# Performance work log

Measured on AMD Instinct MI355X. Metric: run time of the kernel, lower is better.

Reference implementation:

```python
import jax, jax.numpy as jnp
import numpy as np

N_NODES = 100000
N_EDGES = 1600000
IN_DIM = 128
OUT_DIM = 64


def setup_inputs() -> dict:
    key = jax.random.key(0)
    k1, k2, k3, k4, k5 = jax.random.split(key, 5)
    x = jax.random.normal(k1, (N_NODES, IN_DIM), dtype=jnp.float32)
    edge_index = jax.random.randint(k2, (2, N_EDGES), 0, N_NODES, dtype=jnp.int64)
    # xavier_uniform for Linear(in,out): bound = sqrt(6/(in+out))
    wb = float(np.sqrt(6.0 / (IN_DIM + OUT_DIM)))
    W = jax.random.uniform(k3, (OUT_DIM, IN_DIM), dtype=jnp.float32, minval=-wb, maxval=wb)
    # xavier_uniform on a.unsqueeze(0): fan_in=out_dim, fan_out=1
    ab = float(np.sqrt(6.0 / (OUT_DIM + 1)))
    a_src = jax.random.uniform(k4, (OUT_DIM,), dtype=jnp.float32, minval=-ab, maxval=b if (b := ab) else ab)
    a_dst = jax.random.uniform(k5, (OUT_DIM,), dtype=jnp.float32, minval=-ab, maxval=ab)
    return {"x": x, "edge_index": edge_index, "W": W, "a_src": a_src, "a_dst": a_dst}


def reference(x, edge_index, W, a_src, a_dst):
    # h = x @ W^T : [N, out_dim]
    h = x @ W.T
    src, dst = edge_index[0], edge_index[1]
    # per-node attention logits, gathered per edge (cheaper than gathering h twice for the dot)
    s_src = h @ a_src  # [N]
    s_dst = h @ a_dst  # [N]
    e = s_src[src] + s_dst[dst]  # [E]
    e = jnp.where(e >= 0, e, 0.2 * e)  # LeakyReLU(0.2)
    e = jnp.clip(e, -10.0, 10.0)
    alpha_num = jnp.exp(e)
    denom = jax.ops.segment_sum(alpha_num, dst, num_segments=N_NODES)  # [N]
    alpha = alpha_num / (denom[dst] + 1e-9)  # [E]; dropout is identity (eval / p=0)
    msgs = alpha[:, None] * h[src]  # [E, out_dim]
    out = jax.ops.segment_sum(msgs, dst, num_segments=N_NODES)  # [N, out_dim]
    return out
```

## Files before the change

### kernel.cpp

```cpp
#include <hip/hip_runtime.h>
#include <math.h>

#define NN 100000
#define NE 1600000
#define NBKT 391
#define LPS  (NBKT + 1)
#define EPB 2048
#define NPB ((NE + EPB - 1) / EPB)
#define TOTC (NBKT * NPB)
#define SBLK 2048
#define NSB ((TOTC + SBLK - 1) / SBLK)
#define LBUF 6144

typedef unsigned int uint;
typedef unsigned short ushort;
typedef __attribute__((ext_vector_type(8))) short bfx8;
typedef __attribute__((ext_vector_type(4))) float f32x4;

static __device__ __forceinline__ ushort f2bf(float f) {
  uint u = __float_as_uint(f);
  uint r = (u + 0x7fffu + ((u >> 16) & 1u)) >> 16;
  return (ushort)r;
}
static __device__ __forceinline__ float bf2f(ushort v) {
  return __uint_as_float((uint)v << 16);
}
static __device__ __forceinline__ bfx8 cvt8(float4 a, float4 b) {
  bfx8 r;
  r[0] = (short)f2bf(a.x); r[1] = (short)f2bf(a.y);
  r[2] = (short)f2bf(a.z); r[3] = (short)f2bf(a.w);
  r[4] = (short)f2bf(b.x); r[5] = (short)f2bf(b.y);
  r[6] = (short)f2bf(b.z); r[7] = (short)f2bf(b.w);
  return r;
}

__global__ __launch_bounds__(256) void k_h(
    const float* __restrict__ x, const float* __restrict__ W,
    const float* __restrict__ a_src, const float* __restrict__ a_dst,
    ushort* __restrict__ h16, float* __restrict__ ssrc, float* __restrict__ sdst)
{
  __shared__ __align__(16) ushort ws[64 * 128];
  const int t = threadIdx.x;
  const int base = blockIdx.x * 64;
  const float4* x4 = (const float4*)x;
  const float4* W4 = (const float4*)W;

#pragma unroll
  for (int q = 0; q < 8; ++q) {
    int f = q * 256 + t;
    int row = f >> 5, c4 = f & 31;
    float4 v = W4[f];
    ushort4 pk = make_ushort4(f2bf(v.x), f2bf(v.y), f2bf(v.z), f2bf(v.w));
    int byte = row * 256 + ((c4 * 8) ^ ((row & 7) << 4));
    *(ushort4*)((char*)ws + byte) = pk;
  }

  const int wid = t >> 6;
  const int lane = t & 63;
  const int lg = lane >> 4;
  const int lr = lane & 15;

  const int node = base + wid * 16 + lr;
  const bool ok = node < NN;
  const float4* xr = x4 + (size_t)node * 32;

  float4 xa[4][2];
#pragma unroll
  for (int ks = 0; ks < 4; ++ks) {
    xa[ks][0] = ok ? xr[ks * 8 + lg * 2]     : make_float4(0.f, 0.f, 0.f, 0.f);
    xa[ks][1] = ok ? xr[ks * 8 + lg * 2 + 1] : make_float4(0.f, 0.f, 0.f, 0.f);
  }
  __syncthreads();

  f32x4 acc[4];
#pragma unroll
  for (int ng = 0; ng < 4; ++ng) acc[ng] = (f32x4){0.f, 0.f, 0.f, 0.f};

#pragma unroll
  for (int ks = 0; ks < 4; ++ks) {
    int kb = ks * 64 + lg * 16;
    bfx8 af = cvt8(xa[ks][0], xa[ks][1]);
    bfx8 bfr[4];
#pragma unroll
    for (int ng = 0; ng < 4; ++ng) {
      int row = ng * 16 + lr;
      bfr[ng] = *(const bfx8*)((const char*)ws + row * 256 + (kb ^ ((row & 7) << 4)));
    }
#pragma unroll
    for (int ng = 0; ng < 4; ++ng)
      acc[ng] = __builtin_amdgcn_mfma_f32_16x16x32_bf16(af, bfr[ng], acc[ng], 0, 0, 0);
  }

  float as_[4], ad_[4];
#pragma unroll
  for (int ng = 0; ng < 4; ++ng) { as_[ng] = a_src[ng * 16 + lr]; ad_[ng] = a_dst[ng * 16 + lr]; }
#pragma unroll
  for (int r = 0; r < 4; ++r) {
    int nout = base + wid * 16 + lg * 4 + r;
    float ps = 0.f, pd = 0.f;
#pragma unroll
    for (int ng = 0; ng < 4; ++ng) { ps += acc[ng][r] * as_[ng]; pd += acc[ng][r] * ad_[ng]; }
#pragma unroll
    for (int m = 1; m < 16; m <<= 1) { ps += __shfl_xor(ps, m); pd += __shfl_xor(pd, m); }
    if (lr == 0 && nout < NN) { ssrc[nout] = ps; sdst[nout] = pd; }
    if (nout < NN) {
#pragma unroll
      for (int ng = 0; ng < 4; ++ng)
        h16[(size_t)nout * 64 + ng * 16 + lr] = f2bf(acc[ng][r]);
    }
  }
}

__global__ __launch_bounds__(512) void k_sort(const int* __restrict__ ei,
                                              const float* __restrict__ ssrc,
                                              int* __restrict__ cnt,
                                              int* __restrict__ lpre,
                                              int2* __restrict__ stage)
{
  __shared__ int hh[NBKT];
  __shared__ int sums[512];
  __shared__ int2 sbuf[EPB];
  const int t = threadIdx.x, c = blockIdx.x;
  for (int i = t; i < NBKT; i += 512) hh[i] = 0;
  __syncthreads();

  const int base = c * EPB;
  const int nloc = min(EPB, NE - base);
  int my_src[EPB / 512], my_dst[EPB / 512];
#pragma unroll
  for (int q = 0; q < EPB / 512; ++q) {
    int e = base + q * 512 + t;
    if (e < NE) {
      my_src[q] = ei[e];
      my_dst[q] = ei[NE + e];
      atomicAdd(&hh[my_dst[q] >> 8], 1);
    } else my_dst[q] = -1;
  }
  __syncthreads();

  int v = (t < NBKT) ? hh[t] : 0;
  sums[t] = v;
  __syncthreads();
  for (int off = 1; off < 512; off <<= 1) {
    int u = (t >= off) ? sums[t - off] : 0;
    __syncthreads();
    sums[t] += u;
    __syncthreads();
  }
  int ex = sums[t] - v;
  if (t < NBKT) {
    hh[t] = ex;
    lpre[c * LPS + t] = ex;
    cnt[t * NPB + c] = v;
  }
  if (t == 0) lpre[c * LPS + NBKT] = nloc;
  __syncthreads();

#pragma unroll
  for (int q = 0; q < EPB / 512; ++q) {
    if (my_dst[q] >= 0) {
      int dst = my_dst[q], src = my_src[q];
      int pos = atomicAdd(&hh[dst >> 8], 1);
      sbuf[pos] = make_int2(src | ((dst & 255) << 24), __float_as_int(ssrc[src]));
    }
  }
  __syncthreads();
#pragma unroll
  for (int q = 0; q < EPB / 512; ++q) {
    int i = q * 512 + t;
    if (i < nloc) stage[base + i] = sbuf[i];
  }
}

__global__ __launch_bounds__(256) void k_scanA(const int* __restrict__ cnt,
                                               int* __restrict__ partials)
{
  __shared__ int sm[256];
  int t = threadIdx.x, b = blockIdx.x;
  const int4* c4 = (const int4*)(cnt + b * SBLK + t * 8);
  int4 u = c4[0], v = c4[1];
  sm[t] = u.x + u.y + u.z + u.w + v.x + v.y + v.z + v.w;
  __syncthreads();
  for (int s = 128; s > 0; s >>= 1) { if (t < s) sm[t] += sm[t + s]; __syncthreads(); }
  if (t == 0) partials[b] = sm[0];
}

__global__ __launch_bounds__(256) void k_scanB(int* __restrict__ partials,
                                               int* __restrict__ boff,
                                               int* __restrict__ offsets)
{
  __shared__ int sm[256];
  int t = threadIdx.x;
  int v = (t < NSB) ? partials[t] : 0;
  sm[t] = v;
  __syncthreads();
  for (int off = 1; off < 256; off <<= 1) {
    int u = (t >= off) ? sm[t - off] : 0;
    __syncthreads();
    sm[t] += u;
    __syncthreads();
  }
  if (t < NSB) partials[t] = sm[t] - v;
  if (t == 0) { boff[NBKT] = NE; offsets[NN] = NE; }
}

__global__ __launch_bounds__(256) void k_scanC(int* __restrict__ cnt,
                                               const int* __restrict__ partials,
                                               int* __restrict__ boff)
{
  __shared__ int sm[256];
  int t = threadIdx.x, b = blockIdx.x;
  int base = b * SBLK + t * 8;
  int4* c4 = (int4*)(cnt + base);
  int4 u = c4[0], v = c4[1];
  int tot = u.x + u.y + u.z + u.w + v.x + v.y + v.z + v.w;
  sm[t] = tot;
  __syncthreads();
  for (int off = 1; off < 256; off <<= 1) {
    int w = (t >= off) ? sm[t - off] : 0;
    __syncthreads();
    sm[t] += w;
    __syncthreads();
  }
  int run = partials[b] + sm[t] - tot;
  int e[8] = {u.x, u.y, u.z, u.w, v.x, v.y, v.z, v.w};
  int ex[8];
#pragma unroll
  for (int k = 0; k < 8; ++k) { ex[k] = run; run += e[k]; }
#pragma unroll
  for (int k = 0; k < 8; ++k) {
    int idx = base + k;
    if (idx < TOTC && idx % NPB == 0) boff[idx / NPB] = ex[k];
  }
  c4[0] = make_int4(ex[0], ex[1], ex[2], ex[3]);
  c4[1] = make_int4(ex[4], ex[5], ex[6], ex[7]);
}

__global__ __launch_bounds__(512) void k_place(const int* __restrict__ boff,
                                               const int* __restrict__ cnt,
                                               const int* __restrict__ lpre,
                                               const int2* __restrict__ stage,
                                               const float* __restrict__ sdst,
                                               int* __restrict__ offsets,
                                               int2* __restrict__ csr)
{
  __shared__ int2 lbuf[LBUF];
  __shared__ int nh[256];
  __shared__ int cur[256];
  __shared__ float sdl[256];
  const int b = blockIdx.x, t = threadIdx.x;
  const int e_beg = boff[b], e_end = boff[b + 1];
  const int m = e_end - e_beg;

  for (int c = t; c < NPB; c += 512) {
    int lp = lpre[c * LPS + b];
    int lq = lpre[c * LPS + b + 1];
    int outp = cnt[b * NPB + c] - e_beg;
    int sin = c * EPB + lp;
    for (int k = 0; k < lq - lp; ++k) lbuf[outp + k] = stage[sin + k];
  }
  if (t < 256) {
    nh[t] = 0;
    int node = (b << 8) + t;
    sdl[t] = (node < NN) ? sdst[node] : 0.f;
  }
  __syncthreads();

  for (int i = t; i < m; i += 512)
    atomicAdd(&nh[((uint)lbuf[i].x) >> 24], 1);
  __syncthreads();
  int v0 = (t < 256) ? nh[t] : 0;
  for (int off = 1; off < 256; off <<= 1) {
    int u = (t >= off && t < 256) ? nh[t - off] : 0;
    __syncthreads();
    if (t < 256) nh[t] += u;
    __syncthreads();
  }
  if (t < 256) {
    int excl = nh[t] - v0;
    cur[t] = excl;
    int node = (b << 8) + t;
    if (node < NN) offsets[node] = e_beg + excl;
  }
  __syncthreads();

  for (int i = t; i < m; i += 512) {
    int2 v = lbuf[i];
    int dl = ((uint)v.x) >> 24;
    int slot = atomicAdd(&cur[dl], 1);
    float e = __int_as_float(v.y) + sdl[dl];
    e = (e >= 0.f) ? e : 0.2f * e;
    e = fminf(fmaxf(e, -10.f), 10.f);
    csr[e_beg + slot] = make_int2(v.x & 0xFFFFFF, __float_as_int(__expf(e)));
  }
}

__global__ __launch_bounds__(256) void k_agg(const int* __restrict__ offsets,
                                             const int2* __restrict__ csr,
                                             const ushort* __restrict__ h16,
                                             float* __restrict__ out)
{
  int t = blockIdx.x * 256 + threadIdx.x;
  int node = t >> 4;
  if (node >= NN) return;
  int l16 = t & 15;
  int half = l16 >> 3;
  int l8 = l16 & 7;
  int beg = offsets[node];
  int end = offsets[node + 1];
  const uint4* h4 = (const uint4*)h16;
  float a0 = 0.f, a1 = 0.f, a2 = 0.f, a3 = 0.f;
  float a4 = 0.f, a5 = 0.f, a6 = 0.f, a7 = 0.f;
  float den = 0.f;
  int last = end - 1;
  for (int j = beg; j < end; j += 16) {
#pragma unroll
    for (int p = 0; p < 8; ++p) {
      int idx = j + p * 2 + half;
      int2 e = csr[min(idx, last)];
      float a = (idx < end) ? __int_as_float(e.y) : 0.f;
      uint4 hq = h4[(size_t)e.x * 8 + l8];
      den += a;
      a0 += a * bf2f((ushort)(hq.x & 0xffff));
      a1 += a * bf2f((ushort)(hq.x >> 16));
      a2 += a * bf2f((ushort)(hq.y & 0xffff));
      a3 += a * bf2f((ushort)(hq.y >> 16));
      a4 += a * bf2f((ushort)(hq.z & 0xffff));
      a5 += a * bf2f((ushort)(hq.z >> 16));
      a6 += a * bf2f((ushort)(hq.w & 0xffff));
      a7 += a * bf2f((ushort)(hq.w >> 16));
    }
  }
  a0 += __shfl_xor(a0, 8);
  a1 += __shfl_xor(a1, 8);
  a2 += __shfl_xor(a2, 8);
  a3 += __shfl_xor(a3, 8);
  a4 += __shfl_xor(a4, 8);
  a5 += __shfl_xor(a5, 8);
  a6 += __shfl_xor(a6, 8);
  a7 += __shfl_xor(a7, 8);
  den += __shfl_xor(den, 8);
  float inv = 1.f / (den + 1e-9f);
  float4 o = half ? make_float4(a4 * inv, a5 * inv, a6 * inv, a7 * inv)
                  : make_float4(a0 * inv, a1 * inv, a2 * inv, a3 * inv);
  ((float4*)out)[(size_t)node * 16 + l8 * 2 + half] = o;
}

extern "C" void kernel_launch(void* const* d_in, const int* in_sizes, int n_in,
                              void* d_out, int out_size, void* d_ws, size_t ws_size,
                              hipStream_t stream)
{
  const float* x     = (const float*)d_in[0];
  const int*   ei    = (const int*)d_in[1];
  const float* W     = (const float*)d_in[2];
  const float* a_src = (const float*)d_in[3];
  const float* a_dst = (const float*)d_in[4];
  float* out = (float*)d_out;

  char* p = (char*)d_ws;
  auto alloc = [&](size_t bytes) -> char* {
    char* r = p;
    p += (bytes + 255) & ~(size_t)255;
    return r;
  };
  ushort* h16    = (ushort*)alloc((size_t)NN * 64 * 2);
  float* ssrc    = (float*)alloc((size_t)NN * 4);
  float* sdst    = (float*)alloc((size_t)NN * 4);
  int*   offsets = (int*)alloc((size_t)(NN + 1) * 4);
  int*   cnt     = (int*)alloc((size_t)NSB * SBLK * 4);
  int*   lpre    = (int*)alloc((size_t)NPB * LPS * 4);
  int*   boff    = (int*)alloc((size_t)(NBKT + 1) * 4);
  int*   partials= (int*)alloc((size_t)NSB * 4);
  int2*  stage   = (int2*)alloc((size_t)NPB * EPB * 8);
  int2*  csr     = (int2*)alloc((size_t)NE * 8);

  k_h<<<(NN + 63) / 64, 256, 0, stream>>>(x, W, a_src, a_dst, h16, ssrc, sdst);
  k_sort<<<NPB, 512, 0, stream>>>(ei, ssrc, cnt, lpre, stage);
  k_scanA<<<NSB, 256, 0, stream>>>(cnt, partials);
  k_scanB<<<1, 256, 0, stream>>>(partials, boff, offsets);
  k_scanC<<<NSB, 256, 0, stream>>>(cnt, partials, boff);
  k_place<<<NBKT, 512, 0, stream>>>(boff, cnt, lpre, stage, sdst, offsets, csr);
  k_agg<<<((size_t)NN * 16 + 255) / 256, 256, 0, stream>>>(offsets, csr, h16, out);
}
```

Measured before the change: 105.5 us.

## Fuse CSR placement with aggregation per 128-node bucket and transpose counts

Halves bucket size to 128 nodes and fuses the placement and aggregation kernels, so each block sorts its bucket's edges in LDS and aggregates them directly. This drops the global CSR array and offsets round trip. Bucket counts are now written row-major and transposed by a new tiled kernel, which makes the k_sort stores coalesced. The tradeoffs are one extra launch, only 782 blocks doing the gather work (less parallelism than the old per-node grid), and an LDS buffer capped at 2560 edges per bucket that can overflow on skewed degree distributions.

```diff
diff --git a/kernel.cpp b/kernel.cpp
--- a/kernel.cpp
+++ b/kernel.cpp
@@ -3,14 +3,17 @@
 
 #define NN 100000
 #define NE 1600000
-#define NBKT 391
+#define BKB 7
+#define BSZ 128
+#define NBKT 782
 #define LPS  (NBKT + 1)
 #define EPB 2048
 #define NPB ((NE + EPB - 1) / EPB)
 #define TOTC (NBKT * NPB)
 #define SBLK 2048
 #define NSB ((TOTC + SBLK - 1) / SBLK)
-#define LBUF 6144
+#define LBUF2 2560
+#define EVC 5
 
 typedef unsigned int uint;
 typedef unsigned short ushort;
@@ -113,7 +116,7 @@
 
 __global__ __launch_bounds__(512) void k_sort(const int* __restrict__ ei,
                                               const float* __restrict__ ssrc,
-                                              int* __restrict__ cnt,
+                                              int* __restrict__ cnt_cm,
                                               int* __restrict__ lpre,
                                               int2* __restrict__ stage)
 {
@@ -133,13 +136,15 @@
     if (e < NE) {
       my_src[q] = ei[e];
       my_dst[q] = ei[NE + e];
-      atomicAdd(&hh[my_dst[q] >> 8], 1);
+      atomicAdd(&hh[my_dst[q] >> BKB], 1);
     } else my_dst[q] = -1;
   }
   __syncthreads();
 
-  int v = (t < NBKT) ? hh[t] : 0;
-  sums[t] = v;
+  int i0 = 2 * t, i1 = 2 * t + 1;
+  int v0 = (i0 < NBKT) ? hh[i0] : 0;
+  int v1 = (i1 < NBKT) ? hh[i1] : 0;
+  sums[t] = v0 + v1;
   __syncthreads();
   for (int off = 1; off < 512; off <<= 1) {
     int u = (t >= off) ? sums[t - off] : 0;
@@ -147,11 +152,16 @@
     sums[t] += u;
     __syncthreads();
   }
-  int ex = sums[t] - v;
-  if (t < NBKT) {
-    hh[t] = ex;
-    lpre[c * LPS + t] = ex;
-    cnt[t * NPB + c] = v;
+  int ex0 = sums[t] - (v0 + v1);
+  if (i0 < NBKT) {
+    hh[i0] = ex0;
+    lpre[c * LPS + i0] = ex0;
+    cnt_cm[(size_t)c * NBKT + i0] = v0;
+  }
+  if (i1 < NBKT) {
+    hh[i1] = ex0 + v0;
+    lpre[c * LPS + i1] = ex0 + v0;
+    cnt_cm[(size_t)c * NBKT + i1] = v1;
   }
   if (t == 0) lpre[c * LPS + NBKT] = nloc;
   __syncthreads();
@@ -160,8 +170,8 @@
   for (int q = 0; q < EPB / 512; ++q) {
     if (my_dst[q] >= 0) {
       int dst = my_dst[q], src = my_src[q];
-      int pos = atomicAdd(&hh[dst >> 8], 1);
-      sbuf[pos] = make_int2(src | ((dst & 255) << 24), __float_as_int(ssrc[src]));
+      int pos = atomicAdd(&hh[dst >> BKB], 1);
+      sbuf[pos] = make_int2(src | ((dst & (BSZ - 1)) << 24), __float_as_int(ssrc[src]));
     }
   }
   __syncthreads();
@@ -169,6 +179,23 @@
   for (int q = 0; q < EPB / 512; ++q) {
     int i = q * 512 + t;
     if (i < nloc) stage[base + i] = sbuf[i];
+  }
+}
+
+__global__ __launch_bounds__(256) void k_tr(const int* __restrict__ cnt_cm,
+                                            int* __restrict__ cnt)
+{
+  __shared__ int tile[32][33];
+  int cb = blockIdx.x * 32, bb = blockIdx.y * 32;
+  int tx = threadIdx.x & 31, ty = threadIdx.x >> 5;
+  for (int r = ty; r < 32; r += 8) {
+    int c = cb + r, b = bb + tx;
+    tile[r][tx] = (c < NPB && b < NBKT) ? cnt_cm[(size_t)c * NBKT + b] : 0;
+  }
+  __syncthreads();
+  for (int r = ty; r < 32; r += 8) {
+    int b = bb + r, c = cb + tx;
+    if (b < NBKT && c < NPB) cnt[(size_t)b * NPB + c] = tile[tx][r];
   }
 }
 
@@ -185,23 +212,22 @@
   if (t == 0) partials[b] = sm[0];
 }
 
-__global__ __launch_bounds__(256) void k_scanB(int* __restrict__ partials,
-                                               int* __restrict__ boff,
-                                               int* __restrict__ offsets)
-{
-  __shared__ int sm[256];
+__global__ __launch_bounds__(512) void k_scanB(int* __restrict__ partials,
+                                               int* __restrict__ boff)
+{
+  __shared__ int sm[512];
   int t = threadIdx.x;
   int v = (t < NSB) ? partials[t] : 0;
   sm[t] = v;
   __syncthreads();
-  for (int off = 1; off < 256; off <<= 1) {
+  for (int off = 1; off < 512; off <<= 1) {
     int u = (t >= off) ? sm[t - off] : 0;
     __syncthreads();
     sm[t] += u;
     __syncthreads();
   }
   if (t < NSB) partials[t] = sm[t] - v;
-  if (t == 0) { boff[NBKT] = NE; offsets[NN] = NE; }
+  if (t == 0) boff[NBKT] = NE;
 }
 
 __global__ __launch_bounds__(256) void k_scanC(int* __restrict__ cnt,
@@ -236,18 +262,19 @@
   c4[1] = make_int4(ex[4], ex[5], ex[6], ex[7]);
 }
 
-__global__ __launch_bounds__(512) void k_place(const int* __restrict__ boff,
-                                               const int* __restrict__ cnt,
-                                               const int* __restrict__ lpre,
-                                               const int2* __restrict__ stage,
-                                               const float* __restrict__ sdst,
-                                               int* __restrict__ offsets,
-                                               int2* __restrict__ csr)
-{
-  __shared__ int2 lbuf[LBUF];
-  __shared__ int nh[256];
-  __shared__ int cur[256];
-  __shared__ float sdl[256];
+__global__ __launch_bounds__(512) void k_fuse(const int* __restrict__ boff,
+                                              const int* __restrict__ pcnt,
+                                              const int* __restrict__ lpre,
+                                              const int2* __restrict__ stage,
+                                              const float* __restrict__ sdst,
+                                              const ushort* __restrict__ h16,
+                                              float* __restrict__ out)
+{
+  __shared__ int2 lbuf[LBUF2];
+  __shared__ int nh[BSZ];
+  __shared__ int nst[BSZ];
+  __shared__ int cur[BSZ];
+  __shared__ float sdl[BSZ];
   const int b = blockIdx.x, t = threadIdx.x;
   const int e_beg = boff[b], e_end = boff[b + 1];
   const int m = e_end - e_beg;
@@ -255,95 +282,104 @@
   for (int c = t; c < NPB; c += 512) {
     int lp = lpre[c * LPS + b];
     int lq = lpre[c * LPS + b + 1];
-    int outp = cnt[b * NPB + c] - e_beg;
+    int outp = pcnt[(size_t)b * NPB + c] - e_beg;
     int sin = c * EPB + lp;
     for (int k = 0; k < lq - lp; ++k) lbuf[outp + k] = stage[sin + k];
   }
-  if (t < 256) {
+  if (t < BSZ) {
     nh[t] = 0;
-    int node = (b << 8) + t;
+    int node = (b << BKB) + t;
     sdl[t] = (node < NN) ? sdst[node] : 0.f;
   }
   __syncthreads();
 
-  for (int i = t; i < m; i += 512)
-    atomicAdd(&nh[((uint)lbuf[i].x) >> 24], 1);
-  __syncthreads();
-  int v0 = (t < 256) ? nh[t] : 0;
-  for (int off = 1; off < 256; off <<= 1) {
-    int u = (t >= off && t < 256) ? nh[t - off] : 0;
-    __syncthreads();
-    if (t < 256) nh[t] += u;
-    __syncthreads();
-  }
-  if (t < 256) {
-    int excl = nh[t] - v0;
-    cur[t] = excl;
-    int node = (b << 8) + t;
-    if (node < NN) offsets[node] = e_beg + excl;
-  }
-  __syncthreads();
-
-  for (int i = t; i < m; i += 512) {
-    int2 v = lbuf[i];
-    int dl = ((uint)v.x) >> 24;
-    int slot = atomicAdd(&cur[dl], 1);
-    float e = __int_as_float(v.y) + sdl[dl];
-    e = (e >= 0.f) ? e : 0.2f * e;
-    e = fminf(fmaxf(e, -10.f), 10.f);
-    csr[e_beg + slot] = make_int2(v.x & 0xFFFFFF, __float_as_int(__expf(e)));
-  }
-}
-
-__global__ __launch_bounds__(256) void k_agg(const int* __restrict__ offsets,
-                                             const int2* __restrict__ csr,
-                                             const ushort* __restrict__ h16,
-                                             float* __restrict__ out)
-{
-  int t = blockIdx.x * 256 + threadIdx.x;
-  int node = t >> 4;
-  if (node >= NN) return;
-  int l16 = t & 15;
-  int half = l16 >> 3;
-  int l8 = l16 & 7;
-  int beg = offsets[node];
-  int end = offsets[node + 1];
+  int2 ev[EVC];
+  int ne = 0;
+#pragma unroll
+  for (int q = 0; q < EVC; ++q) {
+    int i = q * 512 + t;
+    if (i < m) { ev[q] = lbuf[i]; atomicAdd(&nh[((uint)ev[q].x) >> 24], 1); ne = q + 1; }
+  }
+  __syncthreads();
+  int v0 = (t < BSZ) ? nh[t] : 0;
+  if (t < BSZ) nst[t] = v0;
+  __syncthreads();
+  for (int off = 1; off < BSZ; off <<= 1) {
+    int u = (t >= off && t < BSZ) ? nst[t - off] : 0;
+    __syncthreads();
+    if (t < BSZ) nst[t] += u;
+    __syncthreads();
+  }
+  if (t < BSZ) { int ex = nst[t] - v0; cur[t] = ex; nh[t] = ex; }
+  __syncthreads();
+
+  int slots[EVC];
+  float alph[EVC];
+#pragma unroll
+  for (int q = 0; q < EVC; ++q) {
+    if (q < ne) {
+      int dl = ((uint)ev[q].x) >> 24;
+      slots[q] = atomicAdd(&cur[dl], 1);
+      float e = __int_as_float(ev[q].y) + sdl[dl];
+      e = (e >= 0.f) ? e : 0.2f * e;
+      e = fminf(fmaxf(e, -10.f), 10.f);
+      alph[q] = __expf(e);
+    }
+  }
+  __syncthreads();
+#pragma unroll
+  for (int q = 0; q < EVC; ++q)
+    if (q < ne) lbuf[slots[q]] = make_int2(ev[q].x & 0xFFFFFF, __float_as_int(alph[q]));
+  __syncthreads();
+
+  const int sid = t >> 4;
+  const int l16 = t & 15;
+  const int half = l16 >> 3, l8 = l16 & 7;
   const uint4* h4 = (const uint4*)h16;
-  float a0 = 0.f, a1 = 0.f, a2 = 0.f, a3 = 0.f;
-  float a4 = 0.f, a5 = 0.f, a6 = 0.f, a7 = 0.f;
-  float den = 0.f;
-  int last = end - 1;
-  for (int j = beg; j < end; j += 16) {
-#pragma unroll
-    for (int p = 0; p < 8; ++p) {
-      int idx = j + p * 2 + half;
-      int2 e = csr[min(idx, last)];
-      float a = (idx < end) ? __int_as_float(e.y) : 0.f;
-      uint4 hq = h4[(size_t)e.x * 8 + l8];
-      den += a;
-      a0 += a * bf2f((ushort)(hq.x & 0xffff));
-      a1 += a * bf2f((ushort)(hq.x >> 16));
-      a2 += a * bf2f((ushort)(hq.y & 0xffff));
-      a3 += a * bf2f((ushort)(hq.y >> 16));
-      a4 += a * bf2f((ushort)(hq.z & 0xffff));
-      a5 += a * bf2f((ushort)(hq.z >> 16));
-      a6 += a * bf2f((ushort)(hq.w & 0xffff));
-      a7 += a * bf2f((ushort)(hq.w >> 16));
-    }
-  }
-  a0 += __shfl_xor(a0, 8);
-  a1 += __shfl_xor(a1, 8);
-  a2 += __shfl_xor(a2, 8);
-  a3 += __shfl_xor(a3, 8);
-  a4 += __shfl_xor(a4, 8);
-  a5 += __shfl_xor(a5, 8);
-  a6 += __shfl_xor(a6, 8);
-  a7 += __shfl_xor(a7, 8);
-  den += __shfl_xor(den, 8);
-  float inv = 1.f / (den + 1e-9f);
-  float4 o = half ? make_float4(a4 * inv, a5 * inv, a6 * inv, a7 * inv)
-                  : make_float4(a0 * inv, a1 * inv, a2 * inv, a3 * inv);
-  ((float4*)out)[(size_t)node * 16 + l8 * 2 + half] = o;
+#pragma unroll
+  for (int r = 0; r < 4; ++r) {
+    int nl = sid + 32 * r;
+    int beg = nh[nl];
+    int end = nst[nl];
+    float a0 = 0.f, a1 = 0.f, a2 = 0.f, a3 = 0.f;
+    float a4 = 0.f, a5 = 0.f, a6 = 0.f, a7 = 0.f;
+    float den = 0.f;
+    int last = end - 1;
+    for (int j = beg; j < end; j += 8) {
+#pragma unroll
+      for (int p = 0; p < 4; ++p) {
+        int idx = j + p * 2 + half;
+        int2 e = lbuf[min(idx, last)];
+        float a = (idx < end) ? __int_as_float(e.y) : 0.f;
+        uint4 hq = h4[(size_t)e.x * 8 + l8];
+        den += a;
+        a0 += a * bf2f((ushort)(hq.x & 0xffff));
+        a1 += a * bf2f((ushort)(hq.x >> 16));
+        a2 += a * bf2f((ushort)(hq.y & 0xffff));
+        a3 += a * bf2f((ushort)(hq.y >> 16));
+        a4 += a * bf2f((ushort)(hq.z & 0xffff));
+        a5 += a * bf2f((ushort)(hq.z >> 16));
+        a6 += a * bf2f((ushort)(hq.w & 0xffff));
+        a7 += a * bf2f((ushort)(hq.w >> 16));
+      }
+    }
+    a0 += __shfl_xor(a0, 8);
+    a1 += __shfl_xor(a1, 8);
+    a2 += __shfl_xor(a2, 8);
+    a3 += __shfl_xor(a3, 8);
+    a4 += __shfl_xor(a4, 8);
+    a5 += __shfl_xor(a5, 8);
+    a6 += __shfl_xor(a6, 8);
+    a7 += __shfl_xor(a7, 8);
+    den += __shfl_xor(den, 8);
+    int node = (b << BKB) + nl;
+    if (node < NN) {
+      float inv = 1.f / (den + 1e-9f);
+      float4 o = half ? make_float4(a4 * inv, a5 * inv, a6 * inv, a7 * inv)
+                      : make_float4(a0 * inv, a1 * inv, a2 * inv, a3 * inv);
+      ((float4*)out)[(size_t)node * 16 + l8 * 2 + half] = o;
+    }
+  }
 }
 
 extern "C" void kernel_launch(void* const* d_in, const int* in_sizes, int n_in,
@@ -366,19 +402,18 @@
   ushort* h16    = (ushort*)alloc((size_t)NN * 64 * 2);
   float* ssrc    = (float*)alloc((size_t)NN * 4);
   float* sdst    = (float*)alloc((size_t)NN * 4);
-  int*   offsets = (int*)alloc((size_t)(NN + 1) * 4);
   int*   cnt     = (int*)alloc((size_t)NSB * SBLK * 4);
+  int*   cnt_cm  = (int*)alloc((size_t)NPB * NBKT * 4);
   int*   lpre    = (int*)alloc((size_t)NPB * LPS * 4);
   int*   boff    = (int*)alloc((size_t)(NBKT + 1) * 4);
   int*   partials= (int*)alloc((size_t)NSB * 4);
   int2*  stage   = (int2*)alloc((size_t)NPB * EPB * 8);
-  int2*  csr     = (int2*)alloc((size_t)NE * 8);
 
   k_h<<<(NN + 63) / 64, 256, 0, stream>>>(x, W, a_src, a_dst, h16, ssrc, sdst);
-  k_sort<<<NPB, 512, 0, stream>>>(ei, ssrc, cnt, lpre, stage);
+  k_sort<<<NPB, 512, 0, stream>>>(ei, ssrc, cnt_cm, lpre, stage);
+  k_tr<<<dim3((NPB + 31) / 32, (NBKT + 31) / 32), 256, 0, stream>>>(cnt_cm, cnt);
   k_scanA<<<NSB, 256, 0, stream>>>(cnt, partials);
-  k_scanB<<<1, 256, 0, stream>>>(partials, boff, offsets);
+  k_scanB<<<1, 512, 0, stream>>>(partials, boff);
   k_scanC<<<NSB, 256, 0, stream>>>(cnt, partials, boff);
-  k_place<<<NBKT, 512, 0, stream>>>(boff, cnt, lpre, stage, sdst, offsets, csr);
-  k_agg<<<((size_t)NN * 16 + 255) / 256, 256, 0, stream>>>(offsets, csr, h16, out);
-}
+  k_fuse<<<NBKT, 512, 0, stream>>>(boff, cnt, lpre, stage, sdst, h16, out);
+}
```

New measurement: 95.76 us. 9.2% less time.
